# Performance work log

Hardware: AMD Instinct MI355X
Metric: run time of the kernel (lower is better)

The kernel has to match this reference:

```python
import jax, jax.numpy as jnp
import numpy as np

B, C, DV, HV, WV = 2, 192, 32, 32, 32
S, K, EXP = 16, 4, 2            # d_state, d_conv, expand
DI = EXP * C                     # d_inner = 384
R = (C + 15) // 16               # dt_rank = 12
EPS_LN, EPS_IN = 1e-5, 1e-5


def setup_inputs() -> dict:
    key = jax.random.key(0)
    ks = jax.random.split(key, 16)
    n = lambda k, shp, s=0.02: jax.random.normal(k, shp, dtype=jnp.float32) * s
    A_log = jnp.log(jnp.arange(1, S + 1, dtype=jnp.float32))[None, None, :] * jnp.ones((3, DI, 1), jnp.float32)
    return {
        "x": jax.random.normal(ks[0], (B, C, DV, HV, WV), dtype=jnp.float32),
        "ln_w": jnp.ones((3, C), jnp.float32), "ln_b": jnp.zeros((3, C), jnp.float32),
        "in_w": n(ks[1], (3, 2 * DI, C)),
        "conv_w": n(ks[2], (3, DI, K), 0.1), "conv_b": jnp.zeros((3, DI), jnp.float32),
        "xp_w": n(ks[3], (3, R + 2 * S, DI)),
        "dt_w": n(ks[4], (3, DI, R)), "dt_b": jnp.full((3, DI), -4.0, jnp.float32),
        "A_log": A_log, "Dskip": jnp.ones((3, DI), jnp.float32),
        "out_w": n(ks[5], (3, C, DI)),
        "up_w": n(ks[6], (3, C, C)), "up_b": jnp.zeros((3, C), jnp.float32),
        "Wg_w": n(ks[7], (C, 2 * C)), "Wg_b": jnp.zeros((C,), jnp.float32),
        "Ws_w": n(ks[8], (C, C)), "Ws_b": jnp.zeros((C,), jnp.float32),
        "Wm_w": n(ks[9], (C, C)), "Wm_b": jnp.zeros((C,), jnp.float32),
        "po_w": n(ks[10], (C, 3 * C)), "po_b": jnp.zeros((C,), jnp.float32),
        "res_scale": jnp.float32(1e-3),
    }


def _mamba(seq, iw, cw, cb, xpw, dtw, dtb, Alog, Dsk, ow):
    # seq: (B, L, C) -> (B, L, C); standard Mamba block (selective scan SSM)
    Bb, L, _ = seq.shape
    xm, z = jnp.split(seq @ iw.T, 2, axis=-1)                 # (B,L,DI) each
    # causal depthwise conv1d over L (pad left K-1), then SiLU
    xt = jnp.pad(xm.transpose(0, 2, 1), ((0, 0), (0, 0), (K - 1, 0)))  # (B,DI,L+K-1)
    xc = cb[None, :, None] + sum(cw[:, k][None, :, None] * xt[:, :, k:k + L] for k in range(K))
    xc = jax.nn.silu(xc).transpose(0, 2, 1)                   # (B,L,DI)
    dbc = xc @ xpw.T                                          # (B,L,R+2S)
    dt, Bt, Ct = dbc[..., :R], dbc[..., R:R + S], dbc[..., R + S:]
    dt = jax.nn.softplus(dt @ dtw.T + dtb)                    # (B,L,DI)
    A = -jnp.exp(Alog)                                        # (DI,S)

    def step(h, inp):
        dt_t, b_t, c_t, x_t = inp                             # (B,DI),(B,S),(B,S),(B,DI)
        dA = jnp.exp(dt_t[..., None] * A)                     # (B,DI,S)
        h = dA * h + (dt_t * x_t)[..., None] * b_t[:, None, :]
        return h, jnp.einsum('bds,bs->bd', h, c_t)

    xs = (dt.transpose(1, 0, 2), Bt.transpose(1, 0, 2), Ct.transpose(1, 0, 2), xc.transpose(1, 0, 2))
    _, ys = jax.lax.scan(step, jnp.zeros((Bb, DI, S), seq.dtype), xs)
    y = ys.transpose(1, 0, 2) + Dsk * xc                      # D skip connection
    y = y * jax.nn.silu(z)                                    # gate
    return y @ ow.T                                           # out_proj


def _conv1x1(w, b, v):  # w:(O,C), v:(B,C,D,H,W)
    return jnp.einsum('oc,bcdhw->bodhw', w, v) + b[None, :, None, None, None]


def reference(x, ln_w, ln_b, in_w, conv_w, conv_b, xp_w, dt_w, dt_b, A_log, Dskip,
              out_w, up_w, up_b, Wg_w, Wg_b, Ws_w, Ws_b, Wm_w, Wm_b, po_w, po_b, res_scale):
    red_axes = {0: (3, 4), 1: (2, 4), 2: (2, 3)}  # pool over other two spatial dims
    Zs = []
    for i in range(3):
        seq = x.mean(axis=red_axes[i]).transpose(0, 2, 1)     # (B,L,C), L=D/H/W
        mu = seq.mean(-1, keepdims=True)
        var = seq.var(-1, keepdims=True)
        seq = (seq - mu) / jnp.sqrt(var + EPS_LN) * ln_w[i] + ln_b[i]
        tok = _mamba(seq, in_w[i], conv_w[i], conv_b[i], xp_w[i], dt_w[i], dt_b[i],
                     A_log[i], Dskip[i], out_w[i]).transpose(0, 2, 1)  # (B,C,L)
        if i == 0:
            vol = jnp.broadcast_to(tok[:, :, :, None, None], x.shape)
        elif i == 1:
            vol = jnp.broadcast_to(tok[:, :, None, :, None], x.shape)
        else:
            vol = jnp.broadcast_to(tok[:, :, None, None, :], x.shape)
        Zs.append(_conv1x1(up_w[i], up_b[i], vol))            # up-projection

    def gate(Zi, Zo1, Zo2):
        g = jnp.concatenate([Zo1, Zo2], axis=1).mean(axis=(2, 3, 4))  # GAP(concat(others)) (B,2C)
        ctx = g @ Wg_w.T + Wg_b                                        # (B,C)
        st = _conv1x1(Ws_w, Ws_b, Zi)
        a = jax.nn.relu(ctx[:, :, None, None, None] + st)
        a = jax.nn.sigmoid(_conv1x1(Wm_w, Wm_b, a))
        return a * Zi

    Ya = gate(Zs[0], Zs[1], Zs[2])
    Yc = gate(Zs[1], Zs[0], Zs[2])
    Ys = gate(Zs[2], Zs[0], Zs[1])
    y = _conv1x1(po_w, po_b, jnp.concatenate([Ya, Yc, Ys], axis=1))
    mu = y.mean(axis=(2, 3, 4), keepdims=True)                # InstanceNorm3d (non-affine)
    var = y.var(axis=(2, 3, 4), keepdims=True)
    y = (y - mu) / jnp.sqrt(var + EPS_IN)
    return x + res_scale * y
```

## Files before the change

kernel.cpp:

```cpp
#include <hip/hip_runtime.h>
#include <math.h>

#define BB 2
#define CC 192
#define DI 384
#define SS 16
#define RR 12
#define KK 4

__global__ void k_reduce(const float* __restrict__ x, float* __restrict__ seq) {
  int bc = blockIdx.x; int b = bc / CC, c = bc % CC;
  const float4* xin = (const float4*)(x + (size_t)bc * 32768);
  int t = threadIdx.x;
  int wid = t >> 6;
  __shared__ float pd[32][4];
  __shared__ float swa[256 * 4];
  float hacc = 0.f;
  float4 wacc = {0.f, 0.f, 0.f, 0.f};
  #pragma unroll 8
  for (int k = 0; k < 32; ++k) {
    float4 v = xin[k * 256 + t];
    float s = v.x + v.y + v.z + v.w;
    hacc += s;
    wacc.x += v.x; wacc.y += v.y; wacc.z += v.z; wacc.w += v.w;
    float ss = s;
    #pragma unroll
    for (int off = 32; off > 0; off >>= 1) ss += __shfl_down(ss, off, 64);
    if ((t & 63) == 0) pd[k][wid] = ss;
  }
  #pragma unroll
  for (int off = 4; off > 0; off >>= 1) hacc += __shfl_down(hacc, off, 8);
  if ((t & 7) == 0)
    seq[((1 * BB + b) * 32 + (t >> 3)) * CC + c] = hacc * (1.f / 1024.f);
  ((float4*)swa)[t] = wacc;
  __syncthreads();
  if (t < 32) {
    float s0 = pd[t][0] + pd[t][1] + pd[t][2] + pd[t][3];
    seq[((0 * BB + b) * 32 + t) * CC + c] = s0 * (1.f / 1024.f);
    float s2 = 0.f;
    #pragma unroll
    for (int m = 0; m < 32; ++m) s2 += swa[t + 32 * m];
    seq[((2 * BB + b) * 32 + t) * CC + c] = s2 * (1.f / 1024.f);
  }
}

__global__ void k_lninproj(const float* __restrict__ seq, const float* __restrict__ ln_w,
                           const float* __restrict__ ln_b, const float* __restrict__ in_w,
                           float* __restrict__ xmz) {
  int orig = (blockIdx.x & 7) * 192 + (blockIdx.x >> 3);
  int tok = orig >> 3, chunk = orig & 7;
  int i = tok >> 6;
  int t = threadIdx.x;
  __shared__ float srow[CC];
  __shared__ float sw[3], qw[3];
  __shared__ float pa[192];
  float v = seq[tok * CC + t];
  float s = v, q = v * v;
  #pragma unroll
  for (int off = 32; off > 0; off >>= 1) { s += __shfl_down(s, off, 64); q += __shfl_down(q, off, 64); }
  if ((t & 63) == 0) { sw[t >> 6] = s; qw[t >> 6] = q; }
  __syncthreads();
  float S = sw[0] + sw[1] + sw[2];
  float Q = qw[0] + qw[1] + qw[2];
  float mu = S / CC;
  float var = Q / CC - mu * mu;
  srow[t] = (v - mu) * rsqrtf(var + 1e-5f) * ln_w[i * CC + t] + ln_b[i * CC + t];
  __syncthreads();
  int o = t >> 1, half = t & 1;
  int j = chunk * 96 + o;
  const float4* wr = (const float4*)(in_w + ((size_t)i * 768 + j) * CC);
  const float4* sr = (const float4*)srow;
  float acc = 0.f;
  #pragma unroll 8
  for (int c4 = half * 24; c4 < half * 24 + 24; ++c4) {
    float4 a = wr[c4], bq = sr[c4];
    acc += a.x * bq.x + a.y * bq.y + a.z * bq.z + a.w * bq.w;
  }
  pa[t] = acc;
  __syncthreads();
  if ((t & 1) == 0) xmz[(size_t)tok * 768 + j] = pa[t] + pa[t + 1];
}

__global__ void k_convxp(const float* __restrict__ xmz, const float* __restrict__ conv_w,
                         const float* __restrict__ conv_b, const float* __restrict__ xp_w,
                         float* __restrict__ xc, float* __restrict__ dbc) {
  int tok = blockIdx.x; int l = tok & 31; int tb = tok >> 5; int i = tb / BB;
  int t = threadIdx.x;
  __shared__ float xcl[DI];
  {
    int di = t;
    const float* cw = conv_w + ((size_t)i * DI + di) * KK;
    float acc = conv_b[i * DI + di];
    #pragma unroll
    for (int k = 0; k < KK; ++k) {
      int ls = l + k - 3;
      if (ls >= 0) acc += cw[k] * xmz[(size_t)(tb * 32 + ls) * 768 + di];
    }
    acc = acc / (1.f + expf(-acc));
    xcl[di] = acc;
    xc[(size_t)tok * DI + di] = acc;
  }
  __syncthreads();
  if (t < 352) {
    int o = t >> 3, ln8 = t & 7;
    const float4* wr = (const float4*)(xp_w + ((size_t)i * 44 + o) * DI);
    const float4* xv = (const float4*)xcl;
    float acc = 0.f;
    #pragma unroll
    for (int c4 = ln8 * 12; c4 < ln8 * 12 + 12; ++c4) {
      float4 a = wr[c4], bq = xv[c4];
      acc += a.x * bq.x + a.y * bq.y + a.z * bq.z + a.w * bq.w;
    }
    #pragma unroll
    for (int off = 4; off > 0; off >>= 1) acc += __shfl_xor(acc, off, 8);
    if (ln8 == 0) dbc[tok * 44 + o] = acc;
  }
}

__global__ void k_scan(const float* __restrict__ dbc, const float* __restrict__ xc,
                       const float* __restrict__ xmz, const float* __restrict__ dt_w,
                       const float* __restrict__ dt_b, const float* __restrict__ A_log,
                       const float* __restrict__ Dskip, float* __restrict__ y,
                       float* __restrict__ ymean) {
  int ib = blockIdx.x / 48;
  int di0 = (blockIdx.x % 48) * 8;
  int i = ib / BB;
  int t = threadIdx.x;
  int g = t >> 4, s = t & 15;
  int di = di0 + g;
  __shared__ float sdt[32][8], sxc[32][8], sz[32][8];
  __shared__ float sB[32][SS], sC[32][SS];
  __shared__ float spp[32 * 136];
  __shared__ float sy[32][8];
  __shared__ float sDsk[8];
  #pragma unroll
  for (int j = t; j < 256; j += 128) {
    int l = j >> 3, gg = j & 7;
    int tok = ib * 32 + l;
    sxc[l][gg] = xc[(size_t)tok * DI + di0 + gg];
    sz[l][gg]  = xmz[(size_t)tok * 768 + DI + di0 + gg];
    const float* wr = dt_w + ((size_t)i * DI + di0 + gg) * RR;
    float acc = dt_b[i * DI + di0 + gg];
    #pragma unroll
    for (int r = 0; r < RR; ++r) acc += wr[r] * dbc[tok * 44 + r];
    sdt[l][gg] = (acc > 20.f) ? acc : log1pf(expf(acc));
  }
  #pragma unroll
  for (int j = t; j < 512; j += 128) {
    int l = j >> 4, ss = j & 15;
    sB[l][ss] = dbc[(ib * 32 + l) * 44 + RR + ss];
    sC[l][ss] = dbc[(ib * 32 + l) * 44 + RR + SS + ss];
  }
  if (t < 8) sDsk[t] = Dskip[i * DI + di0 + t];
  float A = -expf(A_log[((size_t)i * DI + di) * SS + s]);
  float h = 0.f;
  __syncthreads();
  #pragma unroll
  for (int l = 0; l < 32; ++l) {
    float dtt = sdt[l][g];
    h = expf(dtt * A) * h + dtt * sxc[l][g] * sB[l][s];
    spp[l * 136 + g * 17 + s] = h * sC[l][s];
  }
  __syncthreads();
  #pragma unroll
  for (int p = 0; p < 2; ++p) {
    int idx = p * 128 + t;
    int l = idx >> 3, g2 = idx & 7;
    float sum = 0.f;
    #pragma unroll
    for (int s2 = 0; s2 < 16; ++s2) sum += spp[l * 136 + g2 * 17 + s2];
    float xt = sxc[l][g2];
    float z  = sz[l][g2];
    float yv = (sum + sDsk[g2] * xt) * (z / (1.f + expf(-z)));
    y[(size_t)(ib * 32 + l) * DI + di0 + g2] = yv;
    sy[l][g2] = yv;
  }
  __syncthreads();
  if (t < 8) {
    float sum = 0.f;
    #pragma unroll
    for (int l = 0; l < 32; ++l) sum += sy[l][t];
    ymean[ib * DI + di0 + t] = sum * (1.f / 32.f);
  }
}

__global__ void k_mz(const float* __restrict__ y, const float* __restrict__ ymean,
                     const float* __restrict__ out_w, const float* __restrict__ up_w,
                     const float* __restrict__ up_b, float* __restrict__ zrow) {
  int j = blockIdx.x;
  int t = threadIdx.x;
  __shared__ float src[DI];
  __shared__ float pa[768];
  __shared__ float mrowL[CC];
  int i = (j < 192) ? (j >> 6) : (j - 192) / BB;
  if (t < DI) src[t] = (j < 192) ? y[(size_t)j * DI + t] : ymean[(j - 192) * DI + t];
  __syncthreads();
  int o = t >> 2, qr = t & 3;
  {
    const float4* wr = (const float4*)(out_w + ((size_t)i * CC + o) * DI);
    const float4* sv = (const float4*)src;
    float acc = 0.f;
    #pragma unroll 8
    for (int c4 = qr * 24; c4 < qr * 24 + 24; ++c4) {
      float4 a = wr[c4], bq = sv[c4];
      acc += a.x * bq.x + a.y * bq.y + a.z * bq.z + a.w * bq.w;
    }
    pa[t] = acc;
  }
  __syncthreads();
  if (t < 192) {
    float4 pv = ((const float4*)pa)[t];
    mrowL[t] = pv.x + pv.y + pv.z + pv.w;
  }
  __syncthreads();
  {
    const float4* ur = (const float4*)(up_w + ((size_t)i * CC + o) * CC);
    const float4* mv = (const float4*)mrowL;
    float acc = 0.f;
    #pragma unroll 8
    for (int c4 = qr * 12; c4 < qr * 12 + 12; ++c4) {
      float4 a = ur[c4], bq = mv[c4];
      acc += a.x * bq.x + a.y * bq.y + a.z * bq.z + a.w * bq.w;
    }
    pa[t] = acc;
  }
  __syncthreads();
  if (t < 192) {
    float4 pv = ((const float4*)pa)[t];
    zrow[(size_t)j * CC + t] = up_b[i * CC + t] + pv.x + pv.y + pv.z + pv.w;
  }
}

__global__ void k_gate(const float* __restrict__ zrow, const float* __restrict__ Wg_w,
                       const float* __restrict__ Wg_b, const float* __restrict__ Ws_w,
                       const float* __restrict__ Ws_b, const float* __restrict__ Wm_w,
                       const float* __restrict__ Wm_b, const float* __restrict__ po_w,
                       float* __restrict__ P) {
  int blk = blockIdx.x; int gb = blk >> 5; int g = gb / BB, b = gb - g * BB;
  int o1 = (g == 0) ? 1 : 0, o2 = (g == 2) ? 1 : 2;
  int t = threadIdx.x;
  __shared__ float zr[CC], zm0[CC], zm1[CC], arow[CC], ygr[CC];
  __shared__ float pa[768], pb[768];
  if (t < CC)            zr[t]        = zrow[(size_t)blk * CC + t];
  else if (t < 2 * CC)   zm0[t - CC]  = zrow[(size_t)(192 + o1 * BB + b) * CC + (t - CC)];
  else if (t < 3 * CC)   zm1[t - 2*CC]= zrow[(size_t)(192 + o2 * BB + b) * CC + (t - 2*CC)];
  __syncthreads();
  int o = t >> 2, qr = t & 3;
  {
    const float4* wr = (const float4*)(Ws_w + (size_t)o * CC);
    const float4* zv = (const float4*)zr;
    float acc = 0.f;
    #pragma unroll 4
    for (int c4 = qr * 12; c4 < qr * 12 + 12; ++c4) {
      float4 a = wr[c4], bq = zv[c4];
      acc += a.x * bq.x + a.y * bq.y + a.z * bq.z + a.w * bq.w;
    }
    pa[t] = acc;
    const float4* gwr = (const float4*)(Wg_w + (size_t)o * 2 * CC);
    float acc2 = 0.f;
    #pragma unroll 4
    for (int c4 = qr * 24; c4 < qr * 24 + 24; ++c4) {
      float4 a = gwr[c4];
      float4 bq = (c4 < 48) ? ((const float4*)zm0)[c4] : ((const float4*)zm1)[c4 - 48];
      acc2 += a.x * bq.x + a.y * bq.y + a.z * bq.z + a.w * bq.w;
    }
    pb[t] = acc2;
  }
  __syncthreads();
  if (t < 192) {
    float4 sa = ((const float4*)pa)[t];
    float4 sb = ((const float4*)pb)[t];
    float a = (Ws_b[t] + sa.x + sa.y + sa.z + sa.w) + (Wg_b[t] + sb.x + sb.y + sb.z + sb.w);
    arow[t] = a > 0.f ? a : 0.f;
  }
  __syncthreads();
  {
    const float4* mr = (const float4*)(Wm_w + (size_t)o * CC);
    const float4* av = (const float4*)arow;
    float acc = 0.f;
    #pragma unroll 4
    for (int c4 = qr * 12; c4 < qr * 12 + 12; ++c4) {
      float4 a = mr[c4], bq = av[c4];
      acc += a.x * bq.x + a.y * bq.y + a.z * bq.z + a.w * bq.w;
    }
    pa[t] = acc;
  }
  __syncthreads();
  if (t < 192) {
    float4 sa = ((const float4*)pa)[t];
    float am = Wm_b[t] + sa.x + sa.y + sa.z + sa.w;
    am = 1.f / (1.f + expf(-am));
    ygr[t] = am * zr[t];
  }
  __syncthreads();
  {
    const float4* pr = (const float4*)(po_w + (size_t)o * (3 * CC) + g * CC);
    const float4* yv = (const float4*)ygr;
    float acc = 0.f;
    #pragma unroll 4
    for (int c4 = qr * 12; c4 < qr * 12 + 12; ++c4) {
      float4 a = pr[c4], bq = yv[c4];
      acc += a.x * bq.x + a.y * bq.y + a.z * bq.z + a.w * bq.w;
    }
    pb[t] = acc;
  }
  __syncthreads();
  if (t < 192) {
    float4 sb = ((const float4*)pb)[t];
    P[(size_t)blk * CC + t] = sb.x + sb.y + sb.z + sb.w;
  }
}

__global__ void k_final(const float* __restrict__ x, const float* __restrict__ P,
                        const float* __restrict__ po_b, const float* __restrict__ rs_p,
                        float* __restrict__ out) {
  int bc = blockIdx.x >> 1; int half = blockIdx.x & 1;
  int b = bc / CC, c = bc % CC;
  __shared__ float p0[32], p1[32], p2[32];
  __shared__ float sbase;
  int t = threadIdx.x;
  if (t < 32) {
    float v0 = P[((0 * BB + b) * 32 + t) * CC + c];
    float v1 = P[((1 * BB + b) * 32 + t) * CC + c];
    float v2 = P[((2 * BB + b) * 32 + t) * CC + c];
    float s0 = v0, q0 = v0 * v0, s1 = v1, q1 = v1 * v1, s2 = v2, q2 = v2 * v2;
    #pragma unroll
    for (int off = 16; off > 0; off >>= 1) {
      s0 += __shfl_xor(s0, off, 32); q0 += __shfl_xor(q0, off, 32);
      s1 += __shfl_xor(s1, off, 32); q1 += __shfl_xor(q1, off, 32);
      s2 += __shfl_xor(s2, off, 32); q2 += __shfl_xor(q2, off, 32);
    }
    float m0 = s0 * (1.f / 32.f), m1 = s1 * (1.f / 32.f), m2 = s2 * (1.f / 32.f);
    float var = (q0 * (1.f / 32.f) - m0 * m0) + (q1 * (1.f / 32.f) - m1 * m1) + (q2 * (1.f / 32.f) - m2 * m2);
    float mu = po_b[c] + m0 + m1 + m2;
    float sc = rs_p[0] * rsqrtf(var + 1e-5f);
    p0[t] = v0 * sc; p1[t] = v1 * sc; p2[t] = v2 * sc;
    if (t == 0) sbase = sc * (po_b[c] - mu);
  }
  __syncthreads();
  float basev = sbase;
  const float4* xin = (const float4*)(x + (size_t)bc * 32768);
  float4* xo = (float4*)(out + (size_t)bc * 32768);
  const float4* p2v = (const float4*)p2;
  int q0i = half * 4096;
  #pragma unroll 4
  for (int q = q0i + t; q < q0i + 4096; q += 256) {
    int d = q >> 8, h = (q >> 3) & 31;
    float add = basev + p0[d] + p1[h];
    float4 pw = p2v[q & 7];
    float4 v = xin[q];
    v.x += add + pw.x;
    v.y += add + pw.y;
    v.z += add + pw.z;
    v.w += add + pw.w;
    xo[q] = v;
  }
}

extern "C" void kernel_launch(void* const* d_in, const int* in_sizes, int n_in,
                              void* d_out, int out_size, void* d_ws, size_t ws_size,
                              hipStream_t stream) {
  const float* x      = (const float*)d_in[0];
  const float* ln_w   = (const float*)d_in[1];
  const float* ln_b   = (const float*)d_in[2];
  const float* in_w   = (const float*)d_in[3];
  const float* conv_w = (const float*)d_in[4];
  const float* conv_b = (const float*)d_in[5];
  const float* xp_w   = (const float*)d_in[6];
  const float* dt_w   = (const float*)d_in[7];
  const float* dt_b   = (const float*)d_in[8];
  const float* A_log  = (const float*)d_in[9];
  const float* Dskip  = (const float*)d_in[10];
  const float* out_w  = (const float*)d_in[11];
  const float* up_w   = (const float*)d_in[12];
  const float* up_b   = (const float*)d_in[13];
  const float* Wg_w   = (const float*)d_in[14];
  const float* Wg_b   = (const float*)d_in[15];
  const float* Ws_w   = (const float*)d_in[16];
  const float* Ws_b   = (const float*)d_in[17];
  const float* Wm_w   = (const float*)d_in[18];
  const float* Wm_b   = (const float*)d_in[19];
  const float* po_w   = (const float*)d_in[20];
  const float* po_b   = (const float*)d_in[21];
  const float* rs_p   = (const float*)d_in[22];
  float* out = (float*)d_out;

  float* ws    = (float*)d_ws;
  float* seq   = ws;
  float* xmz   = seq   + 36864;
  float* xc    = xmz   + 147456;
  float* dbc   = xc    + 73728;
  float* y     = dbc   + 8448;
  float* ymean = y     + 73728;
  float* zrow  = ymean + 2304;
  float* P     = zrow  + 38016;

  k_reduce  <<<dim3(BB * CC),     dim3(256), 0, stream>>>(x, seq);
  k_lninproj<<<dim3(1536),        dim3(192), 0, stream>>>(seq, ln_w, ln_b, in_w, xmz);
  k_convxp  <<<dim3(192),         dim3(384), 0, stream>>>(xmz, conv_w, conv_b, xp_w, xc, dbc);
  k_scan    <<<dim3(288),         dim3(128), 0, stream>>>(dbc, xc, xmz, dt_w, dt_b, A_log,
                                                          Dskip, y, ymean);
  k_mz      <<<dim3(198),         dim3(768), 0, stream>>>(y, ymean, out_w, up_w, up_b, zrow);
  k_gate    <<<dim3(192),         dim3(768), 0, stream>>>(zrow, Wg_w, Wg_b, Ws_w, Ws_b,
                                                          Wm_w, Wm_b, po_w, P);
  k_final   <<<dim3(BB * CC * 2), dim3(256), 0, stream>>>(x, P, po_b, rs_p, out);
}
```

Before: 99.47 us.

## Fuse LayerNorm+in_proj into conv/x_proj kernel, recomputing halo tokens

Merges the LayerNorm/in-projection kernel into the depthwise-conv/x_proj kernel. Each token block now recomputes LayerNorm and the x-half of in_proj for its 3 preceding tokens, so the causal conv reads from shared memory. Only the z-half is written to a smaller global buffer. This removes one launch and the xmz round trip, at the cost of 4x redundant in_proj work on the x-half and fewer blocks (192 vs 1536) doing the matvec.

```diff
diff --git a/kernel.cpp b/kernel.cpp
--- a/kernel.cpp
+++ b/kernel.cpp
@@ -44,58 +44,70 @@
   }
 }
 
-__global__ void k_lninproj(const float* __restrict__ seq, const float* __restrict__ ln_w,
-                           const float* __restrict__ ln_b, const float* __restrict__ in_w,
-                           float* __restrict__ xmz) {
-  int orig = (blockIdx.x & 7) * 192 + (blockIdx.x >> 3);
-  int tok = orig >> 3, chunk = orig & 7;
-  int i = tok >> 6;
-  int t = threadIdx.x;
-  __shared__ float srow[CC];
-  __shared__ float sw[3], qw[3];
-  __shared__ float pa[192];
-  float v = seq[tok * CC + t];
-  float s = v, q = v * v;
-  #pragma unroll
-  for (int off = 32; off > 0; off >>= 1) { s += __shfl_down(s, off, 64); q += __shfl_down(q, off, 64); }
-  if ((t & 63) == 0) { sw[t >> 6] = s; qw[t >> 6] = q; }
-  __syncthreads();
-  float S = sw[0] + sw[1] + sw[2];
-  float Q = qw[0] + qw[1] + qw[2];
-  float mu = S / CC;
-  float var = Q / CC - mu * mu;
-  srow[t] = (v - mu) * rsqrtf(var + 1e-5f) * ln_w[i * CC + t] + ln_b[i * CC + t];
-  __syncthreads();
-  int o = t >> 1, half = t & 1;
-  int j = chunk * 96 + o;
-  const float4* wr = (const float4*)(in_w + ((size_t)i * 768 + j) * CC);
-  const float4* sr = (const float4*)srow;
-  float acc = 0.f;
-  #pragma unroll 8
-  for (int c4 = half * 24; c4 < half * 24 + 24; ++c4) {
-    float4 a = wr[c4], bq = sr[c4];
-    acc += a.x * bq.x + a.y * bq.y + a.z * bq.z + a.w * bq.w;
-  }
-  pa[t] = acc;
-  __syncthreads();
-  if ((t & 1) == 0) xmz[(size_t)tok * 768 + j] = pa[t] + pa[t + 1];
-}
-
-__global__ void k_convxp(const float* __restrict__ xmz, const float* __restrict__ conv_w,
-                         const float* __restrict__ conv_b, const float* __restrict__ xp_w,
-                         float* __restrict__ xc, float* __restrict__ dbc) {
+__global__ void k_convall(const float* __restrict__ seq, const float* __restrict__ ln_w,
+                          const float* __restrict__ ln_b, const float* __restrict__ in_w,
+                          const float* __restrict__ conv_w, const float* __restrict__ conv_b,
+                          const float* __restrict__ xp_w, float* __restrict__ xc,
+                          float* __restrict__ zbuf, float* __restrict__ dbc) {
   int tok = blockIdx.x; int l = tok & 31; int tb = tok >> 5; int i = tb / BB;
   int t = threadIdx.x;
+  __shared__ float sseq[4][CC];
+  __shared__ float smu[4], sri[4];
+  __shared__ float sxm[4][DI];
   __shared__ float xcl[DI];
+  for (int j = t; j < 4 * CC; j += 384) {
+    int k = j / CC, c = j - k * CC;
+    int ls = l - 3 + k;
+    sseq[k][c] = (ls >= 0) ? seq[(tb * 32 + ls) * CC + c] : 0.f;
+  }
+  __syncthreads();
+  int wid = t >> 6, lane = t & 63;
+  if (wid < 4) {
+    float sm = 0.f, sq = 0.f;
+    for (int e = lane; e < CC; e += 64) { float v = sseq[wid][e]; sm += v; sq += v * v; }
+    #pragma unroll
+    for (int off = 32; off > 0; off >>= 1) { sm += __shfl_down(sm, off, 64); sq += __shfl_down(sq, off, 64); }
+    if (lane == 0) { float mu = sm / CC; smu[wid] = mu; sri[wid] = rsqrtf(sq / CC - mu * mu + 1e-5f); }
+  }
+  __syncthreads();
+  for (int j = t; j < 4 * CC; j += 384) {
+    int k = j / CC, c = j - k * CC;
+    sseq[k][c] = (sseq[k][c] - smu[k]) * sri[k] * ln_w[i * CC + c] + ln_b[i * CC + c];
+  }
+  __syncthreads();
+  {
+    const float4* wr = (const float4*)(in_w + ((size_t)i * 768 + t) * CC);
+    const float4* wz = (const float4*)(in_w + ((size_t)i * 768 + 384 + t) * CC);
+    const float4* s0 = (const float4*)sseq[0];
+    const float4* s1 = (const float4*)sseq[1];
+    const float4* s2 = (const float4*)sseq[2];
+    const float4* s3 = (const float4*)sseq[3];
+    float a0 = 0.f, a1 = 0.f, a2 = 0.f, a3 = 0.f, az = 0.f;
+    #pragma unroll 4
+    for (int c4 = 0; c4 < CC / 4; ++c4) {
+      float4 w = wr[c4];
+      float4 q0 = s0[c4], q1 = s1[c4], q2 = s2[c4], q3 = s3[c4];
+      a0 += w.x * q0.x + w.y * q0.y + w.z * q0.z + w.w * q0.w;
+      a1 += w.x * q1.x + w.y * q1.y + w.z * q1.z + w.w * q1.w;
+      a2 += w.x * q2.x + w.y * q2.y + w.z * q2.z + w.w * q2.w;
+      a3 += w.x * q3.x + w.y * q3.y + w.z * q3.z + w.w * q3.w;
+      float4 z = wz[c4];
+      az += z.x * q3.x + z.y * q3.y + z.z * q3.z + z.w * q3.w;
+    }
+    int bl = l - 3;
+    sxm[0][t] = (bl + 0 >= 0) ? a0 : 0.f;
+    sxm[1][t] = (bl + 1 >= 0) ? a1 : 0.f;
+    sxm[2][t] = (bl + 2 >= 0) ? a2 : 0.f;
+    sxm[3][t] = a3;
+    zbuf[(size_t)tok * DI + t] = az;
+  }
+  __syncthreads();
   {
     int di = t;
     const float* cw = conv_w + ((size_t)i * DI + di) * KK;
     float acc = conv_b[i * DI + di];
     #pragma unroll
-    for (int k = 0; k < KK; ++k) {
-      int ls = l + k - 3;
-      if (ls >= 0) acc += cw[k] * xmz[(size_t)(tb * 32 + ls) * 768 + di];
-    }
+    for (int k = 0; k < KK; ++k) acc += cw[k] * sxm[k][di];
     acc = acc / (1.f + expf(-acc));
     xcl[di] = acc;
     xc[(size_t)tok * DI + di] = acc;
@@ -118,7 +130,7 @@
 }
 
 __global__ void k_scan(const float* __restrict__ dbc, const float* __restrict__ xc,
-                       const float* __restrict__ xmz, const float* __restrict__ dt_w,
+                       const float* __restrict__ zbuf, const float* __restrict__ dt_w,
                        const float* __restrict__ dt_b, const float* __restrict__ A_log,
                        const float* __restrict__ Dskip, float* __restrict__ y,
                        float* __restrict__ ymean) {
@@ -138,7 +150,7 @@
     int l = j >> 3, gg = j & 7;
     int tok = ib * 32 + l;
     sxc[l][gg] = xc[(size_t)tok * DI + di0 + gg];
-    sz[l][gg]  = xmz[(size_t)tok * 768 + DI + di0 + gg];
+    sz[l][gg]  = zbuf[(size_t)tok * DI + di0 + gg];
     const float* wr = dt_w + ((size_t)i * DI + di0 + gg) * RR;
     float acc = dt_b[i * DI + di0 + gg];
     #pragma unroll
@@ -387,21 +399,21 @@
 
   float* ws    = (float*)d_ws;
   float* seq   = ws;
-  float* xmz   = seq   + 36864;
-  float* xc    = xmz   + 147456;
-  float* dbc   = xc    + 73728;
+  float* xc    = seq   + 36864;
+  float* zbuf  = xc    + 73728;
+  float* dbc   = zbuf  + 73728;
   float* y     = dbc   + 8448;
   float* ymean = y     + 73728;
   float* zrow  = ymean + 2304;
   float* P     = zrow  + 38016;
 
-  k_reduce  <<<dim3(BB * CC),     dim3(256), 0, stream>>>(x, seq);
-  k_lninproj<<<dim3(1536),        dim3(192), 0, stream>>>(seq, ln_w, ln_b, in_w, xmz);
-  k_convxp  <<<dim3(192),         dim3(384), 0, stream>>>(xmz, conv_w, conv_b, xp_w, xc, dbc);
-  k_scan    <<<dim3(288),         dim3(128), 0, stream>>>(dbc, xc, xmz, dt_w, dt_b, A_log,
-                                                          Dskip, y, ymean);
-  k_mz      <<<dim3(198),         dim3(768), 0, stream>>>(y, ymean, out_w, up_w, up_b, zrow);
-  k_gate    <<<dim3(192),         dim3(768), 0, stream>>>(zrow, Wg_w, Wg_b, Ws_w, Ws_b,
-                                                          Wm_w, Wm_b, po_w, P);
-  k_final   <<<dim3(BB * CC * 2), dim3(256), 0, stream>>>(x, P, po_b, rs_p, out);
-}
+  k_reduce <<<dim3(BB * CC),     dim3(256), 0, stream>>>(x, seq);
+  k_convall<<<dim3(3 * BB * 32), dim3(384), 0, stream>>>(seq, ln_w, ln_b, in_w, conv_w, conv_b,
+                                                         xp_w, xc, zbuf, dbc);
+  k_scan   <<<dim3(288),         dim3(128), 0, stream>>>(dbc, xc, zbuf, dt_w, dt_b, A_log,
+                                                         Dskip, y, ymean);
+  k_mz     <<<dim3(198),         dim3(768), 0, stream>>>(y, ymean, out_w, up_w, up_b, zrow);
+  k_gate   <<<dim3(192),         dim3(768), 0, stream>>>(zrow, Wg_w, Wg_b, Ws_w, Ws_b,
+                                                         Wm_w, Wm_b, po_w, P);
+  k_final  <<<dim3(BB * CC * 2), dim3(256), 0, stream>>>(x, P, po_b, rs_p, out);
+}
```

After: 102.8 us. 1.03x slower.

## Convert linear-layer weights to bf16 inside reduce kernel and consume packed in matvecs

Applied to the files above, without the earlier changes.

The reduce kernel now also converts every linear weight matrix (in_proj, x_proj, out_proj, up, gating and output projections) to bf16 in a workspace buffer. The downstream matvec kernels read the packed bf16 weights as uint4 and unpack them with shifts and masks into fp32 FMAs. This halves weight bytes in later kernels, but every call still reads all fp32 weights once for the conversion and writes the bf16 copy. Weight precision is reduced to bf16, which may affect accuracy.

```diff
diff --git a/kernel.cpp b/kernel.cpp
--- a/kernel.cpp
+++ b/kernel.cpp
@@ -8,7 +8,45 @@
 #define RR 12
 #define KK 4
 
-__global__ void k_reduce(const float* __restrict__ x, float* __restrict__ seq) {
+#define N_IN  442368
+#define N_XP  50688
+#define N_OUT 221184
+#define N_UP  110592
+#define N_WG  73728
+#define N_WS  36864
+#define N_WM  36864
+#define N_PO  110592
+#define O_IN  0
+#define O_XP  442368
+#define O_OUT 493056
+#define O_UP  714240
+#define O_WG  824832
+#define O_WS  898560
+#define O_WM  935424
+#define O_PO  972288
+
+__device__ __forceinline__ unsigned short f2bf(float f) {
+  unsigned int u = __float_as_uint(f);
+  u += 0x7FFFu + ((u >> 16) & 1u);
+  return (unsigned short)(u >> 16);
+}
+
+__device__ __forceinline__ float dot8(uint4 w, const float4* a2) {
+  float4 a0 = a2[0], a1 = a2[1];
+  float s;
+  s  = __uint_as_float(w.x << 16) * a0.x + __uint_as_float(w.x & 0xFFFF0000u) * a0.y;
+  s += __uint_as_float(w.y << 16) * a0.z + __uint_as_float(w.y & 0xFFFF0000u) * a0.w;
+  s += __uint_as_float(w.z << 16) * a1.x + __uint_as_float(w.z & 0xFFFF0000u) * a1.y;
+  s += __uint_as_float(w.w << 16) * a1.z + __uint_as_float(w.w & 0xFFFF0000u) * a1.w;
+  return s;
+}
+
+__global__ void k_reduce(const float* __restrict__ x, float* __restrict__ seq,
+                         const float* __restrict__ in_w, const float* __restrict__ xp_w,
+                         const float* __restrict__ out_w, const float* __restrict__ up_w,
+                         const float* __restrict__ Wg_w, const float* __restrict__ Ws_w,
+                         const float* __restrict__ Wm_w, const float* __restrict__ po_w,
+                         unsigned short* __restrict__ ub) {
   int bc = blockIdx.x; int b = bc / CC, c = bc % CC;
   const float4* xin = (const float4*)(x + (size_t)bc * 32768);
   int t = threadIdx.x;
@@ -42,10 +80,20 @@
     for (int m = 0; m < 32; ++m) s2 += swa[t + 32 * m];
     seq[((2 * BB + b) * 32 + t) * CC + c] = s2 * (1.f / 1024.f);
   }
+  size_t gid = (size_t)bc * 256 + t;
+  const size_t stride = (size_t)BB * CC * 256;
+  for (size_t e = gid; e < N_IN;  e += stride) ub[O_IN  + e] = f2bf(in_w[e]);
+  for (size_t e = gid; e < N_XP;  e += stride) ub[O_XP  + e] = f2bf(xp_w[e]);
+  for (size_t e = gid; e < N_OUT; e += stride) ub[O_OUT + e] = f2bf(out_w[e]);
+  for (size_t e = gid; e < N_UP;  e += stride) ub[O_UP  + e] = f2bf(up_w[e]);
+  for (size_t e = gid; e < N_WG;  e += stride) ub[O_WG  + e] = f2bf(Wg_w[e]);
+  for (size_t e = gid; e < N_WS;  e += stride) ub[O_WS  + e] = f2bf(Ws_w[e]);
+  for (size_t e = gid; e < N_WM;  e += stride) ub[O_WM  + e] = f2bf(Wm_w[e]);
+  for (size_t e = gid; e < N_PO;  e += stride) ub[O_PO  + e] = f2bf(po_w[e]);
 }
 
 __global__ void k_lninproj(const float* __restrict__ seq, const float* __restrict__ ln_w,
-                           const float* __restrict__ ln_b, const float* __restrict__ in_w,
+                           const float* __restrict__ ln_b, const unsigned short* __restrict__ ub,
                            float* __restrict__ xmz) {
   int orig = (blockIdx.x & 7) * 192 + (blockIdx.x >> 3);
   int tok = orig >> 3, chunk = orig & 7;
@@ -68,21 +116,18 @@
   __syncthreads();
   int o = t >> 1, half = t & 1;
   int j = chunk * 96 + o;
-  const float4* wr = (const float4*)(in_w + ((size_t)i * 768 + j) * CC);
+  const uint4* wr = (const uint4*)(ub + O_IN + ((size_t)i * 768 + j) * CC);
   const float4* sr = (const float4*)srow;
   float acc = 0.f;
-  #pragma unroll 8
-  for (int c4 = half * 24; c4 < half * 24 + 24; ++c4) {
-    float4 a = wr[c4], bq = sr[c4];
-    acc += a.x * bq.x + a.y * bq.y + a.z * bq.z + a.w * bq.w;
-  }
+  #pragma unroll
+  for (int u = half * 12; u < half * 12 + 12; ++u) acc += dot8(wr[u], sr + u * 2);
   pa[t] = acc;
   __syncthreads();
   if ((t & 1) == 0) xmz[(size_t)tok * 768 + j] = pa[t] + pa[t + 1];
 }
 
 __global__ void k_convxp(const float* __restrict__ xmz, const float* __restrict__ conv_w,
-                         const float* __restrict__ conv_b, const float* __restrict__ xp_w,
+                         const float* __restrict__ conv_b, const unsigned short* __restrict__ ub,
                          float* __restrict__ xc, float* __restrict__ dbc) {
   int tok = blockIdx.x; int l = tok & 31; int tb = tok >> 5; int i = tb / BB;
   int t = threadIdx.x;
@@ -103,14 +148,11 @@
   __syncthreads();
   if (t < 352) {
     int o = t >> 3, ln8 = t & 7;
-    const float4* wr = (const float4*)(xp_w + ((size_t)i * 44 + o) * DI);
+    const uint4* wr = (const uint4*)(ub + O_XP + ((size_t)i * 44 + o) * DI);
     const float4* xv = (const float4*)xcl;
     float acc = 0.f;
     #pragma unroll
-    for (int c4 = ln8 * 12; c4 < ln8 * 12 + 12; ++c4) {
-      float4 a = wr[c4], bq = xv[c4];
-      acc += a.x * bq.x + a.y * bq.y + a.z * bq.z + a.w * bq.w;
-    }
+    for (int u = ln8 * 6; u < ln8 * 6 + 6; ++u) acc += dot8(wr[u], xv + u * 2);
     #pragma unroll
     for (int off = 4; off > 0; off >>= 1) acc += __shfl_xor(acc, off, 8);
     if (ln8 == 0) dbc[tok * 44 + o] = acc;
@@ -185,8 +227,8 @@
 }
 
 __global__ void k_mz(const float* __restrict__ y, const float* __restrict__ ymean,
-                     const float* __restrict__ out_w, const float* __restrict__ up_w,
-                     const float* __restrict__ up_b, float* __restrict__ zrow) {
+                     const unsigned short* __restrict__ ub, const float* __restrict__ up_b,
+                     float* __restrict__ zrow) {
   int j = blockIdx.x;
   int t = threadIdx.x;
   __shared__ float src[DI];
@@ -197,14 +239,11 @@
   __syncthreads();
   int o = t >> 2, qr = t & 3;
   {
-    const float4* wr = (const float4*)(out_w + ((size_t)i * CC + o) * DI);
+    const uint4* wr = (const uint4*)(ub + O_OUT + ((size_t)i * CC + o) * DI);
     const float4* sv = (const float4*)src;
     float acc = 0.f;
-    #pragma unroll 8
-    for (int c4 = qr * 24; c4 < qr * 24 + 24; ++c4) {
-      float4 a = wr[c4], bq = sv[c4];
-      acc += a.x * bq.x + a.y * bq.y + a.z * bq.z + a.w * bq.w;
-    }
+    #pragma unroll
+    for (int u = qr * 12; u < qr * 12 + 12; ++u) acc += dot8(wr[u], sv + u * 2);
     pa[t] = acc;
   }
   __syncthreads();
@@ -214,14 +253,11 @@
   }
   __syncthreads();
   {
-    const float4* ur = (const float4*)(up_w + ((size_t)i * CC + o) * CC);
+    const uint4* ur = (const uint4*)(ub + O_UP + ((size_t)i * CC + o) * CC);
     const float4* mv = (const float4*)mrowL;
     float acc = 0.f;
-    #pragma unroll 8
-    for (int c4 = qr * 12; c4 < qr * 12 + 12; ++c4) {
-      float4 a = ur[c4], bq = mv[c4];
-      acc += a.x * bq.x + a.y * bq.y + a.z * bq.z + a.w * bq.w;
-    }
+    #pragma unroll
+    for (int u = qr * 6; u < qr * 6 + 6; ++u) acc += dot8(ur[u], mv + u * 2);
     pa[t] = acc;
   }
   __syncthreads();
@@ -231,38 +267,32 @@
   }
 }
 
-__global__ void k_gate(const float* __restrict__ zrow, const float* __restrict__ Wg_w,
-                       const float* __restrict__ Wg_b, const float* __restrict__ Ws_w,
-                       const float* __restrict__ Ws_b, const float* __restrict__ Wm_w,
-                       const float* __restrict__ Wm_b, const float* __restrict__ po_w,
-                       float* __restrict__ P) {
+__global__ void k_gate(const float* __restrict__ zrow, const unsigned short* __restrict__ ub,
+                       const float* __restrict__ Wg_b, const float* __restrict__ Ws_b,
+                       const float* __restrict__ Wm_b, float* __restrict__ P) {
   int blk = blockIdx.x; int gb = blk >> 5; int g = gb / BB, b = gb - g * BB;
   int o1 = (g == 0) ? 1 : 0, o2 = (g == 2) ? 1 : 2;
   int t = threadIdx.x;
   __shared__ float zr[CC], zm0[CC], zm1[CC], arow[CC], ygr[CC];
   __shared__ float pa[768], pb[768];
-  if (t < CC)            zr[t]        = zrow[(size_t)blk * CC + t];
-  else if (t < 2 * CC)   zm0[t - CC]  = zrow[(size_t)(192 + o1 * BB + b) * CC + (t - CC)];
-  else if (t < 3 * CC)   zm1[t - 2*CC]= zrow[(size_t)(192 + o2 * BB + b) * CC + (t - 2*CC)];
+  if (t < CC)            zr[t]         = zrow[(size_t)blk * CC + t];
+  else if (t < 2 * CC)   zm0[t - CC]   = zrow[(size_t)(192 + o1 * BB + b) * CC + (t - CC)];
+  else if (t < 3 * CC)   zm1[t - 2*CC] = zrow[(size_t)(192 + o2 * BB + b) * CC + (t - 2*CC)];
   __syncthreads();
   int o = t >> 2, qr = t & 3;
   {
-    const float4* wr = (const float4*)(Ws_w + (size_t)o * CC);
+    const uint4* wr = (const uint4*)(ub + O_WS + (size_t)o * CC);
     const float4* zv = (const float4*)zr;
     float acc = 0.f;
-    #pragma unroll 4
-    for (int c4 = qr * 12; c4 < qr * 12 + 12; ++c4) {
-      float4 a = wr[c4], bq = zv[c4];
-      acc += a.x * bq.x + a.y * bq.y + a.z * bq.z + a.w * bq.w;
-    }
+    #pragma unroll
+    for (int u = qr * 6; u < qr * 6 + 6; ++u) acc += dot8(wr[u], zv + u * 2);
     pa[t] = acc;
-    const float4* gwr = (const float4*)(Wg_w + (size_t)o * 2 * CC);
+    const uint4* gwr = (const uint4*)(ub + O_WG + (size_t)o * 2 * CC);
     float acc2 = 0.f;
-    #pragma unroll 4
-    for (int c4 = qr * 24; c4 < qr * 24 + 24; ++c4) {
-      float4 a = gwr[c4];
-      float4 bq = (c4 < 48) ? ((const float4*)zm0)[c4] : ((const float4*)zm1)[c4 - 48];
-      acc2 += a.x * bq.x + a.y * bq.y + a.z * bq.z + a.w * bq.w;
+    #pragma unroll
+    for (int u = qr * 12; u < qr * 12 + 12; ++u) {
+      const float4* av = (u < 24) ? ((const float4*)zm0 + u * 2) : ((const float4*)zm1 + (u - 24) * 2);
+      acc2 += dot8(gwr[u], av);
     }
     pb[t] = acc2;
   }
@@ -275,14 +305,11 @@
   }
   __syncthreads();
   {
-    const float4* mr = (const float4*)(Wm_w + (size_t)o * CC);
+    const uint4* mr = (const uint4*)(ub + O_WM + (size_t)o * CC);
     const float4* av = (const float4*)arow;
     float acc = 0.f;
-    #pragma unroll 4
-    for (int c4 = qr * 12; c4 < qr * 12 + 12; ++c4) {
-      float4 a = mr[c4], bq = av[c4];
-      acc += a.x * bq.x + a.y * bq.y + a.z * bq.z + a.w * bq.w;
-    }
+    #pragma unroll
+    for (int u = qr * 6; u < qr * 6 + 6; ++u) acc += dot8(mr[u], av + u * 2);
     pa[t] = acc;
   }
   __syncthreads();
@@ -294,14 +321,11 @@
   }
   __syncthreads();
   {
-    const float4* pr = (const float4*)(po_w + (size_t)o * (3 * CC) + g * CC);
+    const uint4* pr = (const uint4*)(ub + O_PO + (size_t)o * (3 * CC) + (size_t)g * CC);
     const float4* yv = (const float4*)ygr;
     float acc = 0.f;
-    #pragma unroll 4
-    for (int c4 = qr * 12; c4 < qr * 12 + 12; ++c4) {
-      float4 a = pr[c4], bq = yv[c4];
-      acc += a.x * bq.x + a.y * bq.y + a.z * bq.z + a.w * bq.w;
-    }
+    #pragma unroll
+    for (int u = qr * 6; u < qr * 6 + 6; ++u) acc += dot8(pr[u], yv + u * 2);
     pb[t] = acc;
   }
   __syncthreads();
@@ -394,14 +418,15 @@
   float* ymean = y     + 73728;
   float* zrow  = ymean + 2304;
   float* P     = zrow  + 38016;
-
-  k_reduce  <<<dim3(BB * CC),     dim3(256), 0, stream>>>(x, seq);
-  k_lninproj<<<dim3(1536),        dim3(192), 0, stream>>>(seq, ln_w, ln_b, in_w, xmz);
-  k_convxp  <<<dim3(192),         dim3(384), 0, stream>>>(xmz, conv_w, conv_b, xp_w, xc, dbc);
+  unsigned short* ub = (unsigned short*)(ws + 417408);
+
+  k_reduce  <<<dim3(BB * CC),     dim3(256), 0, stream>>>(x, seq, in_w, xp_w, out_w, up_w,
+                                                          Wg_w, Ws_w, Wm_w, po_w, ub);
+  k_lninproj<<<dim3(1536),        dim3(192), 0, stream>>>(seq, ln_w, ln_b, ub, xmz);
+  k_convxp  <<<dim3(192),         dim3(384), 0, stream>>>(xmz, conv_w, conv_b, ub, xc, dbc);
   k_scan    <<<dim3(288),         dim3(128), 0, stream>>>(dbc, xc, xmz, dt_w, dt_b, A_log,
                                                           Dskip, y, ymean);
-  k_mz      <<<dim3(198),         dim3(768), 0, stream>>>(y, ymean, out_w, up_w, up_b, zrow);
-  k_gate    <<<dim3(192),         dim3(768), 0, stream>>>(zrow, Wg_w, Wg_b, Ws_w, Ws_b,
-                                                          Wm_w, Wm_b, po_w, P);
+  k_mz      <<<dim3(198),         dim3(768), 0, stream>>>(y, ymean, ub, up_b, zrow);
+  k_gate    <<<dim3(192),         dim3(768), 0, stream>>>(zrow, ub, Wg_b, Ws_b, Wm_b, P);
   k_final   <<<dim3(BB * CC * 2), dim3(256), 0, stream>>>(x, P, po_b, rs_p, out);
 }
```

Result: faster. 84.18 us (-15.4%).
